# Kernel optimization log

Hardware: AMD Instinct MI355X
Metric: run time of the kernel (lower is better)

Reference implementation:

```python
import jax, jax.numpy as jnp
import numpy as np

SEQ_LEN, IN_DIM = 120, 132
UNITS = (64, 128, 64)
N_LABELS = 101


def _lstm(x, W, U, b):
    """Keras-style LSTM with activation='relu', recurrent_activation='sigmoid'.
    x: (B,T,D), W: (D,4u), U: (u,4u), b: (4u,). Gate order i,f,c,o.
    Returns full hidden sequence (B,T,u)."""
    u = U.shape[0]
    # precompute input projections for all timesteps (big GEMM outside scan)
    xz = jnp.einsum('btd,dz->btz', x, W) + b  # (B,T,4u)

    def step(carry, z_t):
        h, c = carry
        z = z_t + h @ U  # (B,4u)
        i, f, g, o = jnp.split(z, 4, axis=-1)
        i = jax.nn.sigmoid(i)
        f = jax.nn.sigmoid(f)
        o = jax.nn.sigmoid(o)
        c = f * c + i * jax.nn.relu(g)
        h = o * jax.nn.relu(c)
        return (h, c), h

    B = x.shape[0]
    h0 = jnp.zeros((B, u), x.dtype)
    (_, _), hs = jax.lax.scan(step, (h0, h0), jnp.swapaxes(xz, 0, 1))
    return jnp.swapaxes(hs, 0, 1)  # (B,T,u)


def setup_inputs() -> dict:
    key = jax.random.key(0)
    ks = jax.random.split(key, 16)
    s = 0.05
    d = {'x': jax.random.normal(ks[0], (1024, SEQ_LEN, IN_DIM), jnp.float32)}
    in_dims = (IN_DIM,) + UNITS[:-1]
    for l, (din, u) in enumerate(zip(in_dims, UNITS), start=1):
        d[f'W{l}'] = jax.random.normal(ks[3 * l - 2], (din, 4 * u), jnp.float32) * s
        d[f'U{l}'] = jax.random.normal(ks[3 * l - 1], (u, 4 * u), jnp.float32) * s
        d[f'b{l}'] = jnp.zeros((4 * u,), jnp.float32)
    dense_dims = [(UNITS[-1], 64), (64, 32), (32, N_LABELS)]
    for l, (din, dout) in enumerate(dense_dims, start=1):
        d[f'Wd{l}'] = jax.random.normal(ks[9 + l], (din, dout), jnp.float32) * s
        d[f'bd{l}'] = jnp.zeros((dout,), jnp.float32)
    return d


def reference(x, W1, U1, b1, W2, U2, b2, W3, U3, b3,
              Wd1, bd1, Wd2, bd2, Wd3, bd3):
    h = _lstm(x, W1, U1, b1)          # (B,T,64)
    h = _lstm(h, W2, U2, b2)          # (B,T,128)
    h = _lstm(h, W3, U3, b3)[:, -1]   # return_sequences=False -> (B,64)
    h = jax.nn.relu(h @ Wd1 + bd1)    # (B,64)
    h = jax.nn.relu(h @ Wd2 + bd2)    # (B,32)
    return jax.nn.softmax(h @ Wd3 + bd3, axis=-1)  # (B,101)
```

## Files before the change

### kernel.cpp

```cpp
#include <hip/hip_runtime.h>
#include <math.h>

#define T_STEPS 120
#define BATCH   1024

typedef __attribute__((ext_vector_type(8))) short bf16x8;
typedef __attribute__((ext_vector_type(4))) float f32x4;
typedef unsigned short u16;

__device__ __forceinline__ unsigned split2(float f) {
    union { float f; unsigned u; } a; a.f = f;
    unsigned hi = a.u >> 16;
    union { float f; unsigned u; } h; h.u = a.u & 0xFFFF0000u;
    union { float f; unsigned u; } b; b.f = f - h.f;
    unsigned rr = b.u + 0x7FFFu + ((b.u >> 16) & 1);
    return (hi << 16) | (rr >> 16);
}

__device__ __forceinline__ short bf16rne(float f) {
    union { float f; unsigned u; } a; a.f = f;
    unsigned r = a.u + 0x7FFFu + ((a.u >> 16) & 1);
    return (short)(r >> 16);
}

__device__ __forceinline__ float fast_sigmoid(float x) {
    float e = __expf(-x);
    return __builtin_amdgcn_rcpf(1.f + e);
}

__device__ __forceinline__ void block_sync_lds() {
    asm volatile("s_waitcnt lgkmcnt(0)" ::: "memory");
    __builtin_amdgcn_sched_barrier(0);
    __builtin_amdgcn_s_barrier();
    __builtin_amdgcn_sched_barrier(0);
}

__global__ __launch_bounds__(256)
void xconv(const float* __restrict__ x, u16* __restrict__ xhi, u16* __restrict__ xlo)
{
    int idx = blockIdx.x * 256 + threadIdx.x;
    int k   = idx % 144;
    int bt  = idx / 144;
    float f = (k < 132) ? x[(size_t)bt * 132 + k] : 0.f;
    unsigned s = split2(f);
    xhi[idx] = (u16)(s >> 16);
    xlo[idx] = (u16)s;
}

template<int U, int KXD, int KTX, int KTAIL, bool SPLIT, bool LAST_ONLY>
__global__ __launch_bounds__(512, 1)
void lstm_fused(const u16* __restrict__ xhi, const u16* __restrict__ xlo,
                const float* __restrict__ W, int KIN,
                const float* __restrict__ Uw, const float* __restrict__ bias,
                u16* __restrict__ hhi, u16* __restrict__ hlo,
                float* __restrict__ hlast)
{
    constexpr int NZ  = 4 * U;
    constexpr int KTH = U / 32;
    constexpr int NB  = 16;
    constexpr int HPLANE = NB * U;
    constexpr int NGRP = U / 16;
    constexpr int XPSTRIDE = 20;

    __shared__ u16 hsh[4 * HPLANE];
    __shared__ float xp[SPLIT ? 2 * NZ * XPSTRIDE : 4];

    const int tid  = threadIdx.x;
    const int lane = tid & 63;
    const int wid  = tid >> 6;
    const int ln   = lane & 15;
    const int lq   = lane >> 4;
    const bool ish = (!SPLIT) || (wid < NGRP);
    const int g    = SPLIT ? (ish ? wid : wid - NGRP) : wid;
    const int unit = g * 16 + ln;
    const int b0   = blockIdx.x * NB;

    if (ish) {
        bf16x8 bwu[4][KTH];
#pragma unroll
        for (int p = 0; p < 4; ++p)
#pragma unroll
            for (int kt = 0; kt < KTH; ++kt)
#pragma unroll
                for (int e = 0; e < 8; ++e) {
                    int k = kt * 32 + lq * 8 + e;
                    bwu[p][kt][e] = bf16rne(Uw[(size_t)k * NZ + p * U + unit]);
                }
        float breg[4];
#pragma unroll
        for (int p = 0; p < 4; ++p) breg[p] = bias[p * U + unit];

        bf16x8 wxw[KTX][4];
        bf16x8 xfh[KTX], xfl[KTX];
        const u16 *pxh = nullptr, *pxl = nullptr;
        if constexpr (!SPLIT) {
#pragma unroll
            for (int kt = 0; kt < KTX; ++kt)
#pragma unroll
                for (int p = 0; p < 4; ++p)
#pragma unroll
                    for (int e = 0; e < 8; ++e) {
                        int k = kt * 32 + lq * 8 + e;
                        wxw[kt][p][e] = (k < KIN) ? bf16rne(W[(size_t)k * NZ + p * U + unit])
                                                  : (short)0;
                    }
            pxh = xhi + ((size_t)(b0 + ln) * T_STEPS) * KXD + lq * 8;
            pxl = xlo + ((size_t)(b0 + ln) * T_STEPS) * KXD + lq * 8;
#pragma unroll
            for (int kt = 0; kt < KTX; ++kt) {
                xfh[kt] = *reinterpret_cast<const bf16x8*>(pxh + kt * 32);
                xfl[kt] = *reinterpret_cast<const bf16x8*>(pxl + kt * 32);
            }
        }

        u16* hw0 = hsh + ((unit >> 3) * NB + lq * 4) * 8 + (unit & 7);
        u16* hw1 = hw0 + 2 * HPLANE;
        float creg[4];
#pragma unroll
        for (int r = 0; r < 4; ++r) {
            creg[r] = 0.f;
            hw0[r * 8] = 0;
            hw0[HPLANE + r * 8] = 0;
        }

        const u16* hrd[2][KTH];
#pragma unroll
        for (int b = 0; b < 2; ++b)
#pragma unroll
            for (int kt = 0; kt < KTH; ++kt)
                hrd[b][kt] = hsh + b * 2 * HPLANE + ((kt * 4 + lq) * NB + ln) * 8;

        const float* xprd[2];
        xprd[0] = xp + (size_t)0 * NZ * XPSTRIDE;
        xprd[1] = xp + (size_t)1 * NZ * XPSTRIDE;

        size_t ho = ((size_t)(b0 + lq * 4) * T_STEPS) * U + unit;

        block_sync_lds();

#define HSTEP(CUR, OTH, tc)                                                     \
    {                                                                           \
        bf16x8 ahh[KTH], ahl[KTH];                                              \
        _Pragma("unroll")                                                       \
        for (int kt = 0; kt < KTH; ++kt) {                                      \
            ahh[kt] = *reinterpret_cast<const bf16x8*>(hrd[CUR][kt]);           \
            ahl[kt] = *reinterpret_cast<const bf16x8*>(hrd[CUR][kt] + HPLANE);  \
        }                                                                       \
        f32x4 acc[4];                                                           \
        if constexpr (SPLIT) {                                                  \
            _Pragma("unroll")                                                   \
            for (int p = 0; p < 4; ++p) {                                       \
                f32x4 v = *reinterpret_cast<const f32x4*>(                      \
                    xprd[CUR] + (p * U + unit) * XPSTRIDE + lq * 4);            \
                acc[p][0] = v[0] + breg[p]; acc[p][1] = v[1] + breg[p];         \
                acc[p][2] = v[2] + breg[p]; acc[p][3] = v[3] + breg[p];         \
            }                                                                   \
        } else {                                                                \
            _Pragma("unroll")                                                   \
            for (int p = 0; p < 4; ++p) {                                       \
                acc[p][0] = breg[p]; acc[p][1] = breg[p];                       \
                acc[p][2] = breg[p]; acc[p][3] = breg[p];                       \
            }                                                                   \
        }                                                                       \
        _Pragma("unroll")                                                       \
        for (int kt = 0; kt < KTH; ++kt)                                        \
        _Pragma("unroll")                                                       \
        for (int p = 0; p < 4; ++p) {                                           \
            acc[p] = __builtin_amdgcn_mfma_f32_16x16x32_bf16(ahh[kt], bwu[p][kt], acc[p], 0, 0, 0); \
            acc[p] = __builtin_amdgcn_mfma_f32_16x16x32_bf16(ahl[kt], bwu[p][kt], acc[p], 0, 0, 0); \
        }                                                                       \
        if constexpr (!SPLIT) {                                                 \
            _Pragma("unroll")                                                   \
            for (int kt = 0; kt < KTX; ++kt)                                    \
            _Pragma("unroll")                                                   \
            for (int p = 0; p < 4; ++p) {                                       \
                acc[p] = __builtin_amdgcn_mfma_f32_16x16x32_bf16(xfh[kt], wxw[kt][p], acc[p], 0, 0, 0); \
                acc[p] = __builtin_amdgcn_mfma_f32_16x16x32_bf16(xfl[kt], wxw[kt][p], acc[p], 0, 0, 0); \
            }                                                                   \
            if ((tc) + 1 < T_STEPS) {                                           \
                pxh += KXD; pxl += KXD;                                         \
                _Pragma("unroll")                                               \
                for (int kt = 0; kt < KTX; ++kt) {                              \
                    xfh[kt] = *reinterpret_cast<const bf16x8*>(pxh + kt * 32);  \
                    xfl[kt] = *reinterpret_cast<const bf16x8*>(pxl + kt * 32);  \
                }                                                               \
            }                                                                   \
        }                                                                       \
        _Pragma("unroll")                                                       \
        for (int r = 0; r < 4; ++r) {                                           \
            float si = fast_sigmoid(acc[0][r]);                                 \
            float sf = fast_sigmoid(acc[1][r]);                                 \
            float gg = fmaxf(acc[2][r], 0.f);                                   \
            float so = fast_sigmoid(acc[3][r]);                                 \
            float c  = sf * creg[r] + si * gg;                                  \
            creg[r] = c;                                                        \
            float h = so * fmaxf(c, 0.f);                                       \
            unsigned s = split2(h);                                             \
            u16* hw = (OTH) ? hw1 : hw0;                                        \
            hw[r * 8] = (u16)(s >> 16);                                         \
            hw[HPLANE + r * 8] = (u16)s;                                        \
            if constexpr (!LAST_ONLY) {                                         \
                size_t o = ho + (size_t)r * (T_STEPS * U) + (size_t)(tc) * U;   \
                hhi[o] = (u16)(s >> 16);                                        \
                hlo[o] = (u16)s;                                                \
            } else {                                                            \
                if ((tc) == T_STEPS - 1)                                        \
                    hlast[(size_t)(b0 + lq * 4 + r) * U + unit] = h;            \
            }                                                                   \
        }                                                                       \
        block_sync_lds();                                                       \
    }

        for (int t = 0; t < T_STEPS; t += 2) {
            HSTEP(0, 1, t)
            HSTEP(1, 0, t + 1)
        }
#undef HSTEP
    } else {
        bf16x8 wxw[KTX][4];
#pragma unroll
        for (int kt = 0; kt < KTX; ++kt)
#pragma unroll
            for (int p = 0; p < 4; ++p)
#pragma unroll
                for (int e = 0; e < 8; ++e) {
                    int k = kt * 32 + lq * 8 + e;
                    wxw[kt][p][e] = (k < KIN) ? bf16rne(W[(size_t)k * NZ + p * U + unit])
                                              : (short)0;
                }

        const u16* pxh = xhi + ((size_t)(b0 + ln) * T_STEPS) * KXD + lq * 8;
        const u16* pxl = xlo + ((size_t)(b0 + ln) * T_STEPS) * KXD + lq * 8;

        float* xpw[2];
        xpw[0] = xp + (size_t)0 * NZ * XPSTRIDE;
        xpw[1] = xp + (size_t)1 * NZ * XPSTRIDE;

        bf16x8 xfh[KTX] = {}, xfl[KTX] = {};
#pragma unroll
        for (int kt = 0; kt < KTX; ++kt)
            if (kt < KTX - 1 || lq < KTAIL) {
                xfh[kt] = *reinterpret_cast<const bf16x8*>(pxh + kt * 32);
                xfl[kt] = *reinterpret_cast<const bf16x8*>(pxl + kt * 32);
            }

        {
            f32x4 xacc[4] = {};
#pragma unroll
            for (int kt = 0; kt < KTX; ++kt)
#pragma unroll
                for (int p = 0; p < 4; ++p) {
                    xacc[p] = __builtin_amdgcn_mfma_f32_16x16x32_bf16(xfh[kt], wxw[kt][p], xacc[p], 0, 0, 0);
                    xacc[p] = __builtin_amdgcn_mfma_f32_16x16x32_bf16(xfl[kt], wxw[kt][p], xacc[p], 0, 0, 0);
                }
#pragma unroll
            for (int p = 0; p < 4; ++p)
                *reinterpret_cast<f32x4*>(xpw[0] + (p * U + unit) * XPSTRIDE + lq * 4) = xacc[p];
            pxh += KXD; pxl += KXD;
#pragma unroll
            for (int kt = 0; kt < KTX; ++kt)
                if (kt < KTX - 1 || lq < KTAIL) {
                    xfh[kt] = *reinterpret_cast<const bf16x8*>(pxh + kt * 32);
                    xfl[kt] = *reinterpret_cast<const bf16x8*>(pxl + kt * 32);
                }
        }

        block_sync_lds();

#define XSTEP(OTH, tc)                                                          \
    {                                                                           \
        if ((tc) + 1 < T_STEPS) {                                               \
            f32x4 xacc[4] = {};                                                 \
            _Pragma("unroll")                                                   \
            for (int kt = 0; kt < KTX; ++kt)                                    \
            _Pragma("unroll")                                                   \
            for (int p = 0; p < 4; ++p) {                                       \
                xacc[p] = __builtin_amdgcn_mfma_f32_16x16x32_bf16(xfh[kt], wxw[kt][p], xacc[p], 0, 0, 0); \
                xacc[p] = __builtin_amdgcn_mfma_f32_16x16x32_bf16(xfl[kt], wxw[kt][p], xacc[p], 0, 0, 0); \
            }                                                                   \
            _Pragma("unroll")                                                   \
            for (int p = 0; p < 4; ++p)                                         \
                *reinterpret_cast<f32x4*>(xpw[OTH] + (p * U + unit) * XPSTRIDE + lq * 4) = xacc[p]; \
            if ((tc) + 2 < T_STEPS) {                                           \
                pxh += KXD; pxl += KXD;                                         \
                _Pragma("unroll")                                               \
                for (int kt = 0; kt < KTX; ++kt)                                \
                    if (kt < KTX - 1 || lq < KTAIL) {                           \
                        xfh[kt] = *reinterpret_cast<const bf16x8*>(pxh + kt * 32); \
                        xfl[kt] = *reinterpret_cast<const bf16x8*>(pxl + kt * 32); \
                    }                                                           \
            }                                                                   \
        }                                                                       \
        block_sync_lds();                                                       \
    }

        for (int t = 0; t < T_STEPS; t += 2) {
            XSTEP(1, t)
            XSTEP(0, t + 1)
        }
#undef XSTEP
    }
}

__global__ __launch_bounds__(256)
void dense_head(const float* __restrict__ h3,
                const float* __restrict__ Wd1, const float* __restrict__ bd1,
                const float* __restrict__ Wd2, const float* __restrict__ bd2,
                const float* __restrict__ Wd3, const float* __restrict__ bd3,
                float* __restrict__ out)
{
    __shared__ float s1[4][64];
    __shared__ float s2[4][32];
    const int w    = threadIdx.x >> 6;
    const int lane = threadIdx.x & 63;
    const int row  = blockIdx.x * 4 + w;

    float hval = h3[(size_t)row * 64 + lane];
    float a = bd1[lane];
#pragma unroll
    for (int k = 0; k < 64; ++k) {
        float hk = __shfl(hval, k, 64);
        a = fmaf(hk, Wd1[k * 64 + lane], a);
    }
    s1[w][lane] = fmaxf(a, 0.f);
    __syncthreads();

    if (lane < 32) {
        float a2 = bd2[lane];
#pragma unroll
        for (int k = 0; k < 64; ++k) a2 = fmaf(s1[w][k], Wd2[k * 32 + lane], a2);
        s2[w][lane] = fmaxf(a2, 0.f);
    }
    __syncthreads();

    float a0 = bd3[lane];
#pragma unroll
    for (int k = 0; k < 32; ++k) a0 = fmaf(s2[w][k], Wd3[k * 101 + lane], a0);
    float a1 = -INFINITY;
    if (lane < 37) {
        a1 = bd3[64 + lane];
#pragma unroll
        for (int k = 0; k < 32; ++k) a1 = fmaf(s2[w][k], Wd3[k * 101 + 64 + lane], a1);
    }

    float m = fmaxf(a0, a1);
#pragma unroll
    for (int off = 32; off > 0; off >>= 1) m = fmaxf(m, __shfl_xor(m, off, 64));
    float e0 = expf(a0 - m);
    float e1 = (lane < 37) ? expf(a1 - m) : 0.f;
    float s = e0 + e1;
#pragma unroll
    for (int off = 32; off > 0; off >>= 1) s += __shfl_xor(s, off, 64);

    out[(size_t)row * 101 + lane] = e0 / s;
    if (lane < 37) out[(size_t)row * 101 + 64 + lane] = e1 / s;
}

extern "C" void kernel_launch(void* const* d_in, const int* in_sizes, int n_in,
                              void* d_out, int out_size, void* d_ws, size_t ws_size,
                              hipStream_t stream) {
    const float* x   = (const float*)d_in[0];
    const float* W1  = (const float*)d_in[1];
    const float* U1  = (const float*)d_in[2];
    const float* b1  = (const float*)d_in[3];
    const float* W2  = (const float*)d_in[4];
    const float* U2  = (const float*)d_in[5];
    const float* b2  = (const float*)d_in[6];
    const float* W3  = (const float*)d_in[7];
    const float* U3  = (const float*)d_in[8];
    const float* b3  = (const float*)d_in[9];
    const float* Wd1 = (const float*)d_in[10];
    const float* bd1 = (const float*)d_in[11];
    const float* Wd2 = (const float*)d_in[12];
    const float* bd2 = (const float*)d_in[13];
    const float* Wd3 = (const float*)d_in[14];
    const float* bd3 = (const float*)d_in[15];

    u16* ws16 = (u16*)d_ws;
    u16* xhi  = ws16;
    u16* xlo  = xhi + 17694720;
    u16* h2hi = ws16;
    u16* h2lo = h2hi + 15728640;
    u16* h1hi = ws16 + 35389440;
    u16* h1lo = h1hi + 7864320;
    float* h3 = (float*)(ws16 + 51118080);

    xconv<<<(BATCH * T_STEPS * 144) / 256, 256, 0, stream>>>(x, xhi, xlo);
    lstm_fused<64, 144, 5, 2, true, false><<<64, 512, 0, stream>>>(
        xhi, xlo, W1, 132, U1, b1, h1hi, h1lo, nullptr);
    lstm_fused<128, 64, 2, 4, false, false><<<64, 512, 0, stream>>>(
        h1hi, h1lo, W2, 64, U2, b2, h2hi, h2lo, nullptr);
    lstm_fused<64, 128, 4, 4, true, true><<<64, 512, 0, stream>>>(
        h2hi, h2lo, W3, 128, U3, b3, nullptr, nullptr, h3);
    dense_head<<<BATCH / 4, 256, 0, stream>>>(h3, Wd1, bd1, Wd2, bd2, Wd3, bd3,
                                              (float*)d_out);
}
```

Measured before the change: 562.6 us.

## Split layer-2 LSTM into h-waves and x-waves; drop input lo-plane for layer 1

Layer 2 (128 units) previously did both the recurrent and the input-projection MFMAs in the same 8 waves on the serial critical path. It now uses the producer/consumer split already used by layers 1 and 3, with 1024 threads: x-waves precompute the next step's input projection into LDS while h-waves run the recurrence. Separately, layer 1's raw input is converted to a single bf16 plane instead of a hi/lo split, halving conversion writes, input reads and layer-1 x MFMAs. The trade-off is lower precision on the first layer's input projection and higher register and LDS pressure in the larger block.

```diff
diff --git a/kernel.cpp b/kernel.cpp
--- a/kernel.cpp
+++ b/kernel.cpp
@@ -36,19 +36,17 @@
 }
 
 __global__ __launch_bounds__(256)
-void xconv(const float* __restrict__ x, u16* __restrict__ xhi, u16* __restrict__ xlo)
+void xconv(const float* __restrict__ x, u16* __restrict__ xhi)
 {
     int idx = blockIdx.x * 256 + threadIdx.x;
     int k   = idx % 144;
     int bt  = idx / 144;
     float f = (k < 132) ? x[(size_t)bt * 132 + k] : 0.f;
-    unsigned s = split2(f);
-    xhi[idx] = (u16)(s >> 16);
-    xlo[idx] = (u16)s;
-}
-
-template<int U, int KXD, int KTX, int KTAIL, bool SPLIT, bool LAST_ONLY>
-__global__ __launch_bounds__(512, 1)
+    xhi[idx] = (u16)(unsigned short)bf16rne(f);
+}
+
+template<int U, int KXD, int KTX, int KTAIL, int TPB, bool XLO, bool LAST_ONLY>
+__global__ __launch_bounds__(TPB, 1)
 void lstm_fused(const u16* __restrict__ xhi, const u16* __restrict__ xlo,
                 const float* __restrict__ W, int KIN,
                 const float* __restrict__ Uw, const float* __restrict__ bias,
@@ -61,17 +59,18 @@
     constexpr int HPLANE = NB * U;
     constexpr int NGRP = U / 16;
     constexpr int XPSTRIDE = 20;
+    static_assert(TPB == NGRP * 128, "h-waves + x-waves");
 
     __shared__ u16 hsh[4 * HPLANE];
-    __shared__ float xp[SPLIT ? 2 * NZ * XPSTRIDE : 4];
+    __shared__ float xp[2 * NZ * XPSTRIDE];
 
     const int tid  = threadIdx.x;
     const int lane = tid & 63;
     const int wid  = tid >> 6;
     const int ln   = lane & 15;
     const int lq   = lane >> 4;
-    const bool ish = (!SPLIT) || (wid < NGRP);
-    const int g    = SPLIT ? (ish ? wid : wid - NGRP) : wid;
+    const bool ish = (wid < NGRP);
+    const int g    = ish ? wid : wid - NGRP;
     const int unit = g * 16 + ln;
     const int b0   = blockIdx.x * NB;
 
@@ -90,29 +89,6 @@
 #pragma unroll
         for (int p = 0; p < 4; ++p) breg[p] = bias[p * U + unit];
 
-        bf16x8 wxw[KTX][4];
-        bf16x8 xfh[KTX], xfl[KTX];
-        const u16 *pxh = nullptr, *pxl = nullptr;
-        if constexpr (!SPLIT) {
-#pragma unroll
-            for (int kt = 0; kt < KTX; ++kt)
-#pragma unroll
-                for (int p = 0; p < 4; ++p)
-#pragma unroll
-                    for (int e = 0; e < 8; ++e) {
-                        int k = kt * 32 + lq * 8 + e;
-                        wxw[kt][p][e] = (k < KIN) ? bf16rne(W[(size_t)k * NZ + p * U + unit])
-                                                  : (short)0;
-                    }
-            pxh = xhi + ((size_t)(b0 + ln) * T_STEPS) * KXD + lq * 8;
-            pxl = xlo + ((size_t)(b0 + ln) * T_STEPS) * KXD + lq * 8;
-#pragma unroll
-            for (int kt = 0; kt < KTX; ++kt) {
-                xfh[kt] = *reinterpret_cast<const bf16x8*>(pxh + kt * 32);
-                xfl[kt] = *reinterpret_cast<const bf16x8*>(pxl + kt * 32);
-            }
-        }
-
         u16* hw0 = hsh + ((unit >> 3) * NB + lq * 4) * 8 + (unit & 7);
         u16* hw1 = hw0 + 2 * HPLANE;
         float creg[4];
@@ -131,8 +107,8 @@
                 hrd[b][kt] = hsh + b * 2 * HPLANE + ((kt * 4 + lq) * NB + ln) * 8;
 
         const float* xprd[2];
-        xprd[0] = xp + (size_t)0 * NZ * XPSTRIDE;
-        xprd[1] = xp + (size_t)1 * NZ * XPSTRIDE;
+        xprd[0] = xp;
+        xprd[1] = xp + (size_t)NZ * XPSTRIDE;
 
         size_t ho = ((size_t)(b0 + lq * 4) * T_STEPS) * U + unit;
 
@@ -140,50 +116,22 @@
 
 #define HSTEP(CUR, OTH, tc)                                                     \
     {                                                                           \
-        bf16x8 ahh[KTH], ahl[KTH];                                              \
+        f32x4 acc[4];                                                           \
+        _Pragma("unroll")                                                       \
+        for (int p = 0; p < 4; ++p) {                                           \
+            f32x4 v = *reinterpret_cast<const f32x4*>(                          \
+                xprd[CUR] + (p * U + unit) * XPSTRIDE + lq * 4);                \
+            acc[p][0] = v[0] + breg[p]; acc[p][1] = v[1] + breg[p];             \
+            acc[p][2] = v[2] + breg[p]; acc[p][3] = v[3] + breg[p];             \
+        }                                                                       \
         _Pragma("unroll")                                                       \
         for (int kt = 0; kt < KTH; ++kt) {                                      \
-            ahh[kt] = *reinterpret_cast<const bf16x8*>(hrd[CUR][kt]);           \
-            ahl[kt] = *reinterpret_cast<const bf16x8*>(hrd[CUR][kt] + HPLANE);  \
-        }                                                                       \
-        f32x4 acc[4];                                                           \
-        if constexpr (SPLIT) {                                                  \
+            bf16x8 ahh = *reinterpret_cast<const bf16x8*>(hrd[CUR][kt]);        \
+            bf16x8 ahl = *reinterpret_cast<const bf16x8*>(hrd[CUR][kt] + HPLANE); \
             _Pragma("unroll")                                                   \
             for (int p = 0; p < 4; ++p) {                                       \
-                f32x4 v = *reinterpret_cast<const f32x4*>(                      \
-                    xprd[CUR] + (p * U + unit) * XPSTRIDE + lq * 4);            \
-                acc[p][0] = v[0] + breg[p]; acc[p][1] = v[1] + breg[p];         \
-                acc[p][2] = v[2] + breg[p]; acc[p][3] = v[3] + breg[p];         \
-            }                                                                   \
-        } else {                                                                \
-            _Pragma("unroll")                                                   \
-            for (int p = 0; p < 4; ++p) {                                       \
-                acc[p][0] = breg[p]; acc[p][1] = breg[p];                       \
-                acc[p][2] = breg[p]; acc[p][3] = breg[p];                       \
-            }                                                                   \
-        }                                                                       \
-        _Pragma("unroll")                                                       \
-        for (int kt = 0; kt < KTH; ++kt)                                        \
-        _Pragma("unroll")                                                       \
-        for (int p = 0; p < 4; ++p) {                                           \
-            acc[p] = __builtin_amdgcn_mfma_f32_16x16x32_bf16(ahh[kt], bwu[p][kt], acc[p], 0, 0, 0); \
-            acc[p] = __builtin_amdgcn_mfma_f32_16x16x32_bf16(ahl[kt], bwu[p][kt], acc[p], 0, 0, 0); \
-        }                                                                       \
-        if constexpr (!SPLIT) {                                                 \
-            _Pragma("unroll")                                                   \
-            for (int kt = 0; kt < KTX; ++kt)                                    \
-            _Pragma("unroll")                                                   \
-            for (int p = 0; p < 4; ++p) {                                       \
-                acc[p] = __builtin_amdgcn_mfma_f32_16x16x32_bf16(xfh[kt], wxw[kt][p], acc[p], 0, 0, 0); \
-                acc[p] = __builtin_amdgcn_mfma_f32_16x16x32_bf16(xfl[kt], wxw[kt][p], acc[p], 0, 0, 0); \
-            }                                                                   \
-            if ((tc) + 1 < T_STEPS) {                                           \
-                pxh += KXD; pxl += KXD;                                         \
-                _Pragma("unroll")                                               \
-                for (int kt = 0; kt < KTX; ++kt) {                              \
-                    xfh[kt] = *reinterpret_cast<const bf16x8*>(pxh + kt * 32);  \
-                    xfl[kt] = *reinterpret_cast<const bf16x8*>(pxl + kt * 32);  \
-                }                                                               \
+                acc[p] = __builtin_amdgcn_mfma_f32_16x16x32_bf16(ahh, bwu[p][kt], acc[p], 0, 0, 0); \
+                acc[p] = __builtin_amdgcn_mfma_f32_16x16x32_bf16(ahl, bwu[p][kt], acc[p], 0, 0, 0); \
             }                                                                   \
         }                                                                       \
         _Pragma("unroll")                                                       \
@@ -230,18 +178,19 @@
                 }
 
         const u16* pxh = xhi + ((size_t)(b0 + ln) * T_STEPS) * KXD + lq * 8;
-        const u16* pxl = xlo + ((size_t)(b0 + ln) * T_STEPS) * KXD + lq * 8;
+        const u16* pxl = XLO ? (xlo + ((size_t)(b0 + ln) * T_STEPS) * KXD + lq * 8) : nullptr;
 
         float* xpw[2];
-        xpw[0] = xp + (size_t)0 * NZ * XPSTRIDE;
-        xpw[1] = xp + (size_t)1 * NZ * XPSTRIDE;
+        xpw[0] = xp;
+        xpw[1] = xp + (size_t)NZ * XPSTRIDE;
 
         bf16x8 xfh[KTX] = {}, xfl[KTX] = {};
 #pragma unroll
         for (int kt = 0; kt < KTX; ++kt)
             if (kt < KTX - 1 || lq < KTAIL) {
                 xfh[kt] = *reinterpret_cast<const bf16x8*>(pxh + kt * 32);
-                xfl[kt] = *reinterpret_cast<const bf16x8*>(pxl + kt * 32);
+                if constexpr (XLO)
+                    xfl[kt] = *reinterpret_cast<const bf16x8*>(pxl + kt * 32);
             }
 
         {
@@ -251,17 +200,19 @@
 #pragma unroll
                 for (int p = 0; p < 4; ++p) {
                     xacc[p] = __builtin_amdgcn_mfma_f32_16x16x32_bf16(xfh[kt], wxw[kt][p], xacc[p], 0, 0, 0);
-                    xacc[p] = __builtin_amdgcn_mfma_f32_16x16x32_bf16(xfl[kt], wxw[kt][p], xacc[p], 0, 0, 0);
+                    if constexpr (XLO)
+                        xacc[p] = __builtin_amdgcn_mfma_f32_16x16x32_bf16(xfl[kt], wxw[kt][p], xacc[p], 0, 0, 0);
                 }
 #pragma unroll
             for (int p = 0; p < 4; ++p)
                 *reinterpret_cast<f32x4*>(xpw[0] + (p * U + unit) * XPSTRIDE + lq * 4) = xacc[p];
-            pxh += KXD; pxl += KXD;
+            pxh += KXD; if constexpr (XLO) pxl += KXD;
 #pragma unroll
             for (int kt = 0; kt < KTX; ++kt)
                 if (kt < KTX - 1 || lq < KTAIL) {
                     xfh[kt] = *reinterpret_cast<const bf16x8*>(pxh + kt * 32);
-                    xfl[kt] = *reinterpret_cast<const bf16x8*>(pxl + kt * 32);
+                    if constexpr (XLO)
+                        xfl[kt] = *reinterpret_cast<const bf16x8*>(pxl + kt * 32);
                 }
         }
 
@@ -276,18 +227,20 @@
             _Pragma("unroll")                                                   \
             for (int p = 0; p < 4; ++p) {                                       \
                 xacc[p] = __builtin_amdgcn_mfma_f32_16x16x32_bf16(xfh[kt], wxw[kt][p], xacc[p], 0, 0, 0); \
-                xacc[p] = __builtin_amdgcn_mfma_f32_16x16x32_bf16(xfl[kt], wxw[kt][p], xacc[p], 0, 0, 0); \
+                if constexpr (XLO)                                              \
+                    xacc[p] = __builtin_amdgcn_mfma_f32_16x16x32_bf16(xfl[kt], wxw[kt][p], xacc[p], 0, 0, 0); \
             }                                                                   \
             _Pragma("unroll")                                                   \
             for (int p = 0; p < 4; ++p)                                         \
                 *reinterpret_cast<f32x4*>(xpw[OTH] + (p * U + unit) * XPSTRIDE + lq * 4) = xacc[p]; \
             if ((tc) + 2 < T_STEPS) {                                           \
-                pxh += KXD; pxl += KXD;                                         \
+                pxh += KXD; if constexpr (XLO) pxl += KXD;                      \
                 _Pragma("unroll")                                               \
                 for (int kt = 0; kt < KTX; ++kt)                                \
                     if (kt < KTX - 1 || lq < KTAIL) {                           \
                         xfh[kt] = *reinterpret_cast<const bf16x8*>(pxh + kt * 32); \
-                        xfl[kt] = *reinterpret_cast<const bf16x8*>(pxl + kt * 32); \
+                        if constexpr (XLO)                                      \
+                            xfl[kt] = *reinterpret_cast<const bf16x8*>(pxl + kt * 32); \
                     }                                                           \
             }                                                                   \
         }                                                                       \
@@ -378,19 +331,18 @@
 
     u16* ws16 = (u16*)d_ws;
     u16* xhi  = ws16;
-    u16* xlo  = xhi + 17694720;
     u16* h2hi = ws16;
     u16* h2lo = h2hi + 15728640;
     u16* h1hi = ws16 + 35389440;
     u16* h1lo = h1hi + 7864320;
     float* h3 = (float*)(ws16 + 51118080);
 
-    xconv<<<(BATCH * T_STEPS * 144) / 256, 256, 0, stream>>>(x, xhi, xlo);
-    lstm_fused<64, 144, 5, 2, true, false><<<64, 512, 0, stream>>>(
-        xhi, xlo, W1, 132, U1, b1, h1hi, h1lo, nullptr);
-    lstm_fused<128, 64, 2, 4, false, false><<<64, 512, 0, stream>>>(
+    xconv<<<(BATCH * T_STEPS * 144) / 256, 256, 0, stream>>>(x, xhi);
+    lstm_fused<64, 144, 5, 2, 512, false, false><<<64, 512, 0, stream>>>(
+        xhi, nullptr, W1, 132, U1, b1, h1hi, h1lo, nullptr);
+    lstm_fused<128, 64, 2, 4, 1024, true, false><<<64, 1024, 0, stream>>>(
         h1hi, h1lo, W2, 64, U2, b2, h2hi, h2lo, nullptr);
-    lstm_fused<64, 128, 4, 4, true, true><<<64, 512, 0, stream>>>(
+    lstm_fused<64, 128, 4, 4, 512, true, true><<<64, 512, 0, stream>>>(
         h2hi, h2lo, W3, 128, U3, b3, nullptr, nullptr, h3);
     dense_head<<<BATCH / 4, 256, 0, stream>>>(h3, Wd1, bd1, Wd2, bd2, Wd3, bd3,
                                               (float*)d_out);
```

Result: slower. 607.1 us (+7.9%).
